# Optimization experiments

Hardware: AMD Instinct MI355X
Metric: run time of the kernel (lower is better)

Reference implementation:

```python
import jax, jax.numpy as jnp
import numpy as np


def setup_inputs() -> dict:
    key = jax.random.key(0)
    k1, k2, k3, k4 = jax.random.split(key, 4)
    B, S, K, R, DIN, DOUT = 8, 2048, 16, 16, 2048, 2048
    h = jax.random.normal(k1, (B, S, DIN), dtype=jnp.float32)
    alpha = jax.random.uniform(k2, (B, K), dtype=jnp.float32)
    A_bank = jax.random.normal(k3, (K, R, DIN), dtype=jnp.float32) * (1.0 / np.sqrt(DIN))
    B_bank = jax.random.normal(k4, (K, DOUT, R), dtype=jnp.float32) * (1.0 / np.sqrt(R))
    return {"h": h, "alpha": alpha, "A_bank": A_bank, "B_bank": B_bank}


def reference(h, alpha, A_bank, B_bank):
    # Mix K low-rank bases per sample, then apply low-rank delta to h.
    A_mixed = jnp.einsum('bk,kri->bri', alpha, A_bank)   # [B, r, d_in]
    B_mixed = jnp.einsum('bk,kor->bor', alpha, B_bank)   # [B, d_out, r]
    z = jnp.einsum('bri,bsi->bsr', A_mixed, h)           # [B, S, r]
    delta = jnp.einsum('bor,bsr->bso', B_mixed, z)       # [B, S, d_out]
    return delta
```

## Files before the change

### kernel.cpp

```cpp
#include <hip/hip_runtime.h>

typedef unsigned int u32;
typedef float f32x4 __attribute__((ext_vector_type(4)));

#define BB 8
#define SS 2048
#define KK 16
#define RR 16
#define DIN 2048
#define DOUT 2048

__global__ void __launch_bounds__(256) mix_kernel(
    const float* __restrict__ alpha,
    const float* __restrict__ A_bank,
    const float* __restrict__ B_bank,
    float* __restrict__ Am,
    float* __restrict__ Bm)
{
    int t = blockIdx.x * 256 + threadIdx.x;
    const int half = BB * RR * DIN;
    if (t < half) {
        int i = t & (DIN - 1);
        int r = (t >> 11) & (RR - 1);
        int b = t >> 15;
        float acc = 0.f;
#pragma unroll
        for (int k = 0; k < KK; ++k)
            acc += alpha[b * KK + k] * A_bank[(k * RR + r) * DIN + i];
        Am[t] = acc;
    } else {
        int u = t - half;
        int r = u & (RR - 1);
        int o = (u >> 4) & (DOUT - 1);
        int b = u >> 15;
        float acc = 0.f;
#pragma unroll
        for (int k = 0; k < KK; ++k)
            acc += alpha[b * KK + k] * B_bank[(k * DOUT + o) * RR + r];
        Bm[u] = acc;
    }
}

__global__ void __launch_bounds__(256, 3) z_kernel(
    const float* __restrict__ h,
    const float* __restrict__ Am,
    float* __restrict__ z)
{
    int b = blockIdx.y;
    int wid = threadIdx.x >> 6;
    int lane = threadIdx.x & 63;
    int s0 = blockIdx.x * 16 + wid * 4;
    const float* hb = h + (size_t)b * SS * DIN + (size_t)s0 * DIN;
    const float* Ab = Am + (size_t)b * RR * DIN;

    float a[64];
#pragma unroll
    for (int v = 0; v < 64; ++v) a[v] = 0.f;

#pragma unroll 1
    for (int t = 0; t < 8; ++t) {
        int i0 = t * 256 + lane * 4;
        float4 hv0 = *(const float4*)(hb + i0);
        float4 hv1 = *(const float4*)(hb + DIN + i0);
        float4 hv2 = *(const float4*)(hb + 2 * DIN + i0);
        float4 hv3 = *(const float4*)(hb + 3 * DIN + i0);
#pragma unroll
        for (int r = 0; r < 16; ++r) {
            float4 av = *(const float4*)(Ab + r * DIN + i0);
            a[0 * 16 + r] += hv0.x * av.x + hv0.y * av.y + hv0.z * av.z + hv0.w * av.w;
            a[1 * 16 + r] += hv1.x * av.x + hv1.y * av.y + hv1.z * av.z + hv1.w * av.w;
            a[2 * 16 + r] += hv2.x * av.x + hv2.y * av.y + hv2.z * av.z + hv2.w * av.w;
            a[3 * 16 + r] += hv3.x * av.x + hv3.y * av.y + hv3.z * av.z + hv3.w * av.w;
        }
    }

#pragma unroll
    for (int off = 32; off >= 1; off >>= 1) {
        bool up = (lane & off) != 0;
#pragma unroll
        for (int v = 0; v < off; ++v) {
            float send = up ? a[v] : a[v + off];
            float keep = up ? a[v + off] : a[v];
            a[v] = keep + __shfl_xor(send, off, 64);
        }
    }
    z[(size_t)(b * SS + s0) * RR + lane] = a[0];
}

__global__ void __launch_bounds__(256, 4) delta_kernel(
    const float* __restrict__ z,
    const float* __restrict__ Bm,
    float* __restrict__ out)
{
    int b = blockIdx.z;
    int s0 = blockIdx.y * 64;
    int o0 = blockIdx.x * 1024 + threadIdx.x * 4;

    const float* wp = Bm + ((size_t)b * DOUT + o0) * RR;
    float w[4][16];
#pragma unroll
    for (int j = 0; j < 4; ++j) {
#pragma unroll
        for (int q = 0; q < 4; ++q) {
            float4 p = *(const float4*)(wp + j * 16 + q * 4);
            w[j][q * 4 + 0] = p.x; w[j][q * 4 + 1] = p.y;
            w[j][q * 4 + 2] = p.z; w[j][q * 4 + 3] = p.w;
        }
    }

    const float* zp = z + (size_t)(b * SS + s0) * RR;
    float* op = out + ((size_t)b * SS + s0) * DOUT + o0;

#pragma unroll 2
    for (int s = 0; s < 64; ++s) {
        float4 z0 = *(const float4*)(zp + s * 16);
        float4 z1 = *(const float4*)(zp + s * 16 + 4);
        float4 z2 = *(const float4*)(zp + s * 16 + 8);
        float4 z3 = *(const float4*)(zp + s * 16 + 12);
        float zz[16] = {z0.x, z0.y, z0.z, z0.w, z1.x, z1.y, z1.z, z1.w,
                        z2.x, z2.y, z2.z, z2.w, z3.x, z3.y, z3.z, z3.w};
        float rj[4];
#pragma unroll
        for (int j = 0; j < 4; ++j) {
            float acc = 0.f;
#pragma unroll
            for (int r = 0; r < 16; ++r) acc += w[j][r] * zz[r];
            rj[j] = acc;
        }
        f32x4 res;
        res.x = rj[0]; res.y = rj[1]; res.z = rj[2]; res.w = rj[3];
        __builtin_nontemporal_store(res, (f32x4*)(op + (size_t)s * DOUT));
    }
}

extern "C" void kernel_launch(void* const* d_in, const int* in_sizes, int n_in,
                              void* d_out, int out_size, void* d_ws, size_t ws_size,
                              hipStream_t stream)
{
    const float* h      = (const float*)d_in[0];
    const float* alpha  = (const float*)d_in[1];
    const float* A_bank = (const float*)d_in[2];
    const float* B_bank = (const float*)d_in[3];
    float* out = (float*)d_out;

    float* Am = (float*)d_ws;
    float* Bm = Am + BB * RR * DIN;
    float* z  = Bm + BB * DOUT * RR;

    mix_kernel<<<2048, 256, 0, stream>>>(alpha, A_bank, B_bank, Am, Bm);
    z_kernel<<<dim3(128, 8), 256, 0, stream>>>(h, Am, z);
    delta_kernel<<<dim3(2, 32, 8), 256, 0, stream>>>(z, Bm, out);
}
```

Baseline: 257.0 us.

## Fuse z projection and delta expansion into one kernel via shared memory

Merges the z and delta kernels: each block computes z for 16 sequence rows, stages it in shared memory, then expands it to the full output width for those rows. The z round trip through global memory and one launch go away, and the read-h and write-out phases can overlap across blocks. In exchange each block reloads its B_mixed weights for every 16-row tile instead of every 64 rows, and launch bounds rise to 4 waves per SIMD, which may pressure the register-heavy z accumulation. The h loads are also marked nontemporal.

```diff
diff --git a/kernel.cpp b/kernel.cpp
--- a/kernel.cpp
+++ b/kernel.cpp
@@ -41,16 +41,21 @@
     }
 }
 
-__global__ void __launch_bounds__(256, 3) z_kernel(
+__global__ void __launch_bounds__(256, 4) zdelta_kernel(
     const float* __restrict__ h,
     const float* __restrict__ Am,
-    float* __restrict__ z)
+    const float* __restrict__ Bm,
+    float* __restrict__ out)
 {
+    __shared__ float zl[16 * 16];
+
     int b = blockIdx.y;
     int wid = threadIdx.x >> 6;
     int lane = threadIdx.x & 63;
-    int s0 = blockIdx.x * 16 + wid * 4;
-    const float* hb = h + (size_t)b * SS * DIN + (size_t)s0 * DIN;
+    int stile = blockIdx.x * 16;
+    int s0 = stile + wid * 4;
+
+    const float* hb = h + ((size_t)b * SS + s0) * DIN;
     const float* Ab = Am + (size_t)b * RR * DIN;
 
     float a[64];
@@ -60,13 +65,13 @@
 #pragma unroll 1
     for (int t = 0; t < 8; ++t) {
         int i0 = t * 256 + lane * 4;
-        float4 hv0 = *(const float4*)(hb + i0);
-        float4 hv1 = *(const float4*)(hb + DIN + i0);
-        float4 hv2 = *(const float4*)(hb + 2 * DIN + i0);
-        float4 hv3 = *(const float4*)(hb + 3 * DIN + i0);
+        f32x4 hv0 = __builtin_nontemporal_load((const f32x4*)(hb + i0));
+        f32x4 hv1 = __builtin_nontemporal_load((const f32x4*)(hb + DIN + i0));
+        f32x4 hv2 = __builtin_nontemporal_load((const f32x4*)(hb + 2 * DIN + i0));
+        f32x4 hv3 = __builtin_nontemporal_load((const f32x4*)(hb + 3 * DIN + i0));
 #pragma unroll
         for (int r = 0; r < 16; ++r) {
-            float4 av = *(const float4*)(Ab + r * DIN + i0);
+            f32x4 av = *(const f32x4*)(Ab + r * DIN + i0);
             a[0 * 16 + r] += hv0.x * av.x + hv0.y * av.y + hv0.z * av.z + hv0.w * av.w;
             a[1 * 16 + r] += hv1.x * av.x + hv1.y * av.y + hv1.z * av.z + hv1.w * av.w;
             a[2 * 16 + r] += hv2.x * av.x + hv2.y * av.y + hv2.z * av.z + hv2.w * av.w;
@@ -84,52 +89,46 @@
             a[v] = keep + __shfl_xor(send, off, 64);
         }
     }
-    z[(size_t)(b * SS + s0) * RR + lane] = a[0];
-}
+    zl[(wid * 4 + (lane >> 4)) * 16 + (lane & 15)] = a[0];
+    __syncthreads();
 
-__global__ void __launch_bounds__(256, 4) delta_kernel(
-    const float* __restrict__ z,
-    const float* __restrict__ Bm,
-    float* __restrict__ out)
-{
-    int b = blockIdx.z;
-    int s0 = blockIdx.y * 64;
-    int o0 = blockIdx.x * 1024 + threadIdx.x * 4;
-
-    const float* wp = Bm + ((size_t)b * DOUT + o0) * RR;
-    float w[4][16];
-#pragma unroll
-    for (int j = 0; j < 4; ++j) {
-#pragma unroll
-        for (int q = 0; q < 4; ++q) {
-            float4 p = *(const float4*)(wp + j * 16 + q * 4);
-            w[j][q * 4 + 0] = p.x; w[j][q * 4 + 1] = p.y;
-            w[j][q * 4 + 2] = p.z; w[j][q * 4 + 3] = p.w;
-        }
-    }
-
-    const float* zp = z + (size_t)(b * SS + s0) * RR;
-    float* op = out + ((size_t)b * SS + s0) * DOUT + o0;
-
-#pragma unroll 2
-    for (int s = 0; s < 64; ++s) {
-        float4 z0 = *(const float4*)(zp + s * 16);
-        float4 z1 = *(const float4*)(zp + s * 16 + 4);
-        float4 z2 = *(const float4*)(zp + s * 16 + 8);
-        float4 z3 = *(const float4*)(zp + s * 16 + 12);
-        float zz[16] = {z0.x, z0.y, z0.z, z0.w, z1.x, z1.y, z1.z, z1.w,
-                        z2.x, z2.y, z2.z, z2.w, z3.x, z3.y, z3.z, z3.w};
-        float rj[4];
+    int tx = threadIdx.x;
+#pragma unroll 1
+    for (int ot = 0; ot < 2; ++ot) {
+        int o0 = ot * 1024 + tx * 4;
+        const float* wp = Bm + ((size_t)b * DOUT + o0) * RR;
+        float w[4][16];
 #pragma unroll
         for (int j = 0; j < 4; ++j) {
-            float acc = 0.f;
 #pragma unroll
-            for (int r = 0; r < 16; ++r) acc += w[j][r] * zz[r];
-            rj[j] = acc;
+            for (int q = 0; q < 4; ++q) {
+                f32x4 p = *(const f32x4*)(wp + j * 16 + q * 4);
+                w[j][q * 4 + 0] = p.x; w[j][q * 4 + 1] = p.y;
+                w[j][q * 4 + 2] = p.z; w[j][q * 4 + 3] = p.w;
+            }
         }
-        f32x4 res;
-        res.x = rj[0]; res.y = rj[1]; res.z = rj[2]; res.w = rj[3];
-        __builtin_nontemporal_store(res, (f32x4*)(op + (size_t)s * DOUT));
+
+        float* op = out + ((size_t)b * SS + stile) * DOUT + o0;
+#pragma unroll 2
+        for (int s = 0; s < 16; ++s) {
+            f32x4 z0 = *(const f32x4*)(&zl[s * 16 + 0]);
+            f32x4 z1 = *(const f32x4*)(&zl[s * 16 + 4]);
+            f32x4 z2 = *(const f32x4*)(&zl[s * 16 + 8]);
+            f32x4 z3 = *(const f32x4*)(&zl[s * 16 + 12]);
+            float zz[16] = {z0.x, z0.y, z0.z, z0.w, z1.x, z1.y, z1.z, z1.w,
+                            z2.x, z2.y, z2.z, z2.w, z3.x, z3.y, z3.z, z3.w};
+            float rj[4];
+#pragma unroll
+            for (int j = 0; j < 4; ++j) {
+                float acc = 0.f;
+#pragma unroll
+                for (int r = 0; r < 16; ++r) acc += w[j][r] * zz[r];
+                rj[j] = acc;
+            }
+            f32x4 res;
+            res.x = rj[0]; res.y = rj[1]; res.z = rj[2]; res.w = rj[3];
+            __builtin_nontemporal_store(res, (f32x4*)(op + (size_t)s * DOUT));
+        }
     }
 }
 
@@ -145,9 +144,7 @@
 
     float* Am = (float*)d_ws;
     float* Bm = Am + BB * RR * DIN;
-    float* z  = Bm + BB * DOUT * RR;
 
     mix_kernel<<<2048, 256, 0, stream>>>(alpha, A_bank, B_bank, Am, Bm);
-    z_kernel<<<dim3(128, 8), 256, 0, stream>>>(h, Am, z);
-    delta_kernel<<<dim3(2, 32, 8), 256, 0, stream>>>(z, Bm, out);
+    zdelta_kernel<<<dim3(128, 8), 256, 0, stream>>>(h, Am, Bm, out);
 }
```

After: 258.6 us. About the same (+0.6%).
